# Kernel tuning notes

Hardware: AMD Instinct MI355X
Metric: run time of the kernel (lower is better)

The kernel has to match this reference:

```python
import jax, jax.numpy as jnp
import numpy as np

N, C = 16384, 4096
MARGIN = 0.1


def setup_inputs() -> dict:
    key = jax.random.key(0)
    k1, k2 = jax.random.split(key)
    cossim = jax.random.normal(k1, (N, C), dtype=jnp.float32)
    correct = jax.random.randint(k2, (N,), 0, C)
    target = jax.nn.one_hot(correct, C, dtype=jnp.int32)  # one-hot [N, C]
    return {"cossim": cossim, "target": target}


def reference(cossim, target):
    # correct column per row (target is one-hot)
    correct_idx = jnp.argmax(target, axis=1)  # [N]
    correct_sim = jnp.take_along_axis(cossim, correct_idx[:, None], axis=1)  # [N, 1]
    # hinge = clamp(margin + sim - correct_sim, min=0), excluding the correct column
    hinge = jnp.maximum(MARGIN + cossim - correct_sim, 0.0)  # [N, C]
    is_correct = target == 1
    hinge = jnp.where(is_correct, 0.0, hinge)
    loss = jnp.sum(hinge) / N
    return loss
```

## Files before the change

kernel.cpp:

```cpp
#include <hip/hip_runtime.h>

#define N_ROWS 16384
#define N_COLS 4096
#define MARGIN 0.1f
#define BLOCK  256
#define RPB    2
#define NBLOCKS (N_ROWS / RPB)

typedef float vf4 __attribute__((ext_vector_type(4)));
typedef int   vi4 __attribute__((ext_vector_type(4)));

__global__ __launch_bounds__(BLOCK) void
mm_row_kernel(const float* __restrict__ cossim,
              const int* __restrict__ target,
              float* __restrict__ partials) {
    const int t = threadIdx.x;
    const size_t r0 = (size_t)blockIdx.x * RPB;

    vf4 c[RPB][4];
    vi4 tg[RPB][4];
#pragma unroll
    for (int r = 0; r < RPB; ++r) {
        const vf4* __restrict__ cos4 = (const vf4*)(cossim + (r0 + r) * N_COLS);
        const vi4* __restrict__ tgt4 = (const vi4*)(target + (r0 + r) * N_COLS);
#pragma unroll
        for (int k = 0; k < 4; ++k) {
            c[r][k]  = cos4[t + k * BLOCK];
            tg[r][k] = tgt4[t + k * BLOCK];
        }
    }

    __shared__ float s_cs[RPB];
#pragma unroll
    for (int r = 0; r < RPB; ++r)
#pragma unroll
        for (int k = 0; k < 4; ++k)
#pragma unroll
            for (int j = 0; j < 4; ++j)
                if (tg[r][k][j] == 1) s_cs[r] = c[r][k][j];
    __syncthreads();

    float acc = 0.0f;
#pragma unroll
    for (int r = 0; r < RPB; ++r) {
        const float mc = MARGIN - s_cs[r];
#pragma unroll
        for (int k = 0; k < 4; ++k)
#pragma unroll
            for (int j = 0; j < 4; ++j)
                acc += fmaxf(mc + c[r][k][j], 0.0f);
    }

#pragma unroll
    for (int off = 32; off > 0; off >>= 1)
        acc += __shfl_down(acc, off, 64);

    __shared__ float s_wave[BLOCK / 64];
    const int lane = t & 63, wave = t >> 6;
    if (lane == 0) s_wave[wave] = acc;
    __syncthreads();
    if (t == 0) {
        float s = s_wave[0] + s_wave[1] + s_wave[2] + s_wave[3];
        partials[blockIdx.x] = s - (float)RPB * MARGIN;
    }
}

__global__ __launch_bounds__(BLOCK) void
mm_reduce_kernel(const float* __restrict__ partials, float* __restrict__ out) {
    const int t = threadIdx.x;
    float acc = 0.0f;
    for (int i = t; i < NBLOCKS; i += BLOCK) acc += partials[i];
#pragma unroll
    for (int off = 32; off > 0; off >>= 1)
        acc += __shfl_down(acc, off, 64);
    __shared__ float s_wave[BLOCK / 64];
    const int lane = t & 63, wave = t >> 6;
    if (lane == 0) s_wave[wave] = acc;
    __syncthreads();
    if (t == 0) {
        out[0] = (s_wave[0] + s_wave[1] + s_wave[2] + s_wave[3]) * (1.0f / N_ROWS);
    }
}

extern "C" void kernel_launch(void* const* d_in, const int* in_sizes, int n_in,
                              void* d_out, int out_size, void* d_ws, size_t ws_size,
                              hipStream_t stream) {
    const float* cossim = (const float*)d_in[0];
    const int*   target = (const int*)d_in[1];
    float* out      = (float*)d_out;
    float* partials = (float*)d_ws;

    mm_row_kernel<<<NBLOCKS, BLOCK, 0, stream>>>(cossim, target, partials);
    mm_reduce_kernel<<<1, BLOCK, 0, stream>>>(partials, out);
}
```

Measured before the change: 506.6 us.

## Split row kernel into separate find-correct and hinge-sum kernels

Splits the fused per-row kernel into three kernels: one scans the one-hot target and writes each row's correct similarity to a table, one streams cossim to compute hinge sums, and the existing final reduction. Rows are now handled one per block, and the margin correction moves into the final reduce. This drops the shared-memory handoff and block barrier inside the row kernel and shrinks register use per kernel. The cost is an extra launch and a serialized pass over the target array before cossim is read, where the fused kernel overlapped the two streams.

```diff
diff --git a/kernel.cpp b/kernel.cpp
--- a/kernel.cpp
+++ b/kernel.cpp
@@ -4,52 +4,53 @@
 #define N_COLS 4096
 #define MARGIN 0.1f
 #define BLOCK  256
-#define RPB    2
-#define NBLOCKS (N_ROWS / RPB)
 
 typedef float vf4 __attribute__((ext_vector_type(4)));
 typedef int   vi4 __attribute__((ext_vector_type(4)));
 
 __global__ __launch_bounds__(BLOCK) void
-mm_row_kernel(const float* __restrict__ cossim,
-              const int* __restrict__ target,
-              float* __restrict__ partials) {
-    const int t = threadIdx.x;
-    const size_t r0 = (size_t)blockIdx.x * RPB;
+mm_find_kernel(const int* __restrict__ target,
+               const float* __restrict__ cossim,
+               float* __restrict__ cs_table) {
+    const int row = blockIdx.x;
+    const int t   = threadIdx.x;
+    const vi4* __restrict__ tgt4 = (const vi4*)(target + (size_t)row * N_COLS);
 
-    vf4 c[RPB][4];
-    vi4 tg[RPB][4];
+    vi4 tg[4];
 #pragma unroll
-    for (int r = 0; r < RPB; ++r) {
-        const vf4* __restrict__ cos4 = (const vf4*)(cossim + (r0 + r) * N_COLS);
-        const vi4* __restrict__ tgt4 = (const vi4*)(target + (r0 + r) * N_COLS);
+    for (int k = 0; k < 4; ++k) tg[k] = tgt4[t + k * BLOCK];
+
 #pragma unroll
-        for (int k = 0; k < 4; ++k) {
-            c[r][k]  = cos4[t + k * BLOCK];
-            tg[r][k] = tgt4[t + k * BLOCK];
+    for (int k = 0; k < 4; ++k) {
+#pragma unroll
+        for (int j = 0; j < 4; ++j) {
+            if (tg[k][j] == 1) {
+                const int col = (t + k * BLOCK) * 4 + j;
+                cs_table[row] = cossim[(size_t)row * N_COLS + col];
+            }
         }
     }
+}
 
-    __shared__ float s_cs[RPB];
+__global__ __launch_bounds__(BLOCK) void
+mm_hinge_kernel(const float* __restrict__ cossim,
+                const float* __restrict__ cs_table,
+                float* __restrict__ partials) {
+    const int row = blockIdx.x;
+    const int t   = threadIdx.x;
+    const float mc = MARGIN - cs_table[row];
+    const vf4* __restrict__ cos4 = (const vf4*)(cossim + (size_t)row * N_COLS);
+
+    vf4 c[4];
 #pragma unroll
-    for (int r = 0; r < RPB; ++r)
-#pragma unroll
-        for (int k = 0; k < 4; ++k)
-#pragma unroll
-            for (int j = 0; j < 4; ++j)
-                if (tg[r][k][j] == 1) s_cs[r] = c[r][k][j];
-    __syncthreads();
+    for (int k = 0; k < 4; ++k) c[k] = cos4[t + k * BLOCK];
 
     float acc = 0.0f;
 #pragma unroll
-    for (int r = 0; r < RPB; ++r) {
-        const float mc = MARGIN - s_cs[r];
+    for (int k = 0; k < 4; ++k)
 #pragma unroll
-        for (int k = 0; k < 4; ++k)
-#pragma unroll
-            for (int j = 0; j < 4; ++j)
-                acc += fmaxf(mc + c[r][k][j], 0.0f);
-    }
+        for (int j = 0; j < 4; ++j)
+            acc += fmaxf(mc + c[k][j], 0.0f);
 
 #pragma unroll
     for (int off = 32; off > 0; off >>= 1)
@@ -59,17 +60,15 @@
     const int lane = t & 63, wave = t >> 6;
     if (lane == 0) s_wave[wave] = acc;
     __syncthreads();
-    if (t == 0) {
-        float s = s_wave[0] + s_wave[1] + s_wave[2] + s_wave[3];
-        partials[blockIdx.x] = s - (float)RPB * MARGIN;
-    }
+    if (t == 0)
+        partials[row] = s_wave[0] + s_wave[1] + s_wave[2] + s_wave[3];
 }
 
 __global__ __launch_bounds__(BLOCK) void
 mm_reduce_kernel(const float* __restrict__ partials, float* __restrict__ out) {
     const int t = threadIdx.x;
     float acc = 0.0f;
-    for (int i = t; i < NBLOCKS; i += BLOCK) acc += partials[i];
+    for (int i = t; i < N_ROWS; i += BLOCK) acc += partials[i];
 #pragma unroll
     for (int off = 32; off > 0; off >>= 1)
         acc += __shfl_down(acc, off, 64);
@@ -77,9 +76,9 @@
     const int lane = t & 63, wave = t >> 6;
     if (lane == 0) s_wave[wave] = acc;
     __syncthreads();
-    if (t == 0) {
-        out[0] = (s_wave[0] + s_wave[1] + s_wave[2] + s_wave[3]) * (1.0f / N_ROWS);
-    }
+    if (t == 0)
+        out[0] = (s_wave[0] + s_wave[1] + s_wave[2] + s_wave[3]) * (1.0f / N_ROWS)
+                 - MARGIN;
 }
 
 extern "C" void kernel_launch(void* const* d_in, const int* in_sizes, int n_in,
@@ -88,8 +87,10 @@
     const float* cossim = (const float*)d_in[0];
     const int*   target = (const int*)d_in[1];
     float* out      = (float*)d_out;
-    float* partials = (float*)d_ws;
+    float* cs_table = (float*)d_ws;
+    float* partials = (float*)d_ws + N_ROWS;
 
-    mm_row_kernel<<<NBLOCKS, BLOCK, 0, stream>>>(cossim, target, partials);
+    mm_find_kernel<<<N_ROWS, BLOCK, 0, stream>>>(target, cossim, cs_table);
+    mm_hinge_kernel<<<N_ROWS, BLOCK, 0, stream>>>(cossim, cs_table, partials);
     mm_reduce_kernel<<<1, BLOCK, 0, stream>>>(partials, out);
 }
```

New measurement: 502.6 us. Within noise of the previous version (-0.8%).
